# Kernel optimization log

Measured on AMD Instinct MI355X. Metric: run time of the kernel, lower is better.

Reference implementation:

```python
import jax, jax.numpy as jnp
import numpy as np

N, E, G = 100000, 1600000, 2048
F_NODE, F_EDGE, H, T = 32, 8, 128, 12


def _lin(key, fan_in, fan_out):
    k1, k2 = jax.random.split(key)
    s = 1.0 / np.sqrt(fan_in)
    W = jax.random.uniform(k1, (fan_in, fan_out), jnp.float32, -s, s)
    b = jax.random.uniform(k2, (fan_out,), jnp.float32, -s, s)
    return W, b


def setup_inputs() -> dict:
    key = jax.random.key(0)
    ks = jax.random.split(key, 12)
    x = jax.random.normal(ks[0], (N, F_NODE), jnp.float32)
    edge_index = jax.random.randint(ks[1], (2, E), 0, N, jnp.int64)
    edge_attr = jax.random.normal(ks[2], (E, F_EDGE), jnp.float32)
    batch = jnp.sort(jax.random.randint(ks[3], (N,), 0, G, jnp.int64))
    We1, be1 = _lin(ks[4], F_EDGE, F_NODE)   # conv1 edge lin: edge_dim -> in_channels
    W1a, b1a = _lin(ks[5], F_NODE, H)
    W1b, b1b = _lin(ks[6], H, H)
    We2, be2 = _lin(ks[7], F_EDGE, H)        # conv2 edge lin: edge_dim -> hidden
    W2a, b2a = _lin(ks[8], H, H)
    W2b, b2b = _lin(ks[9], H, H)
    Wl1, bl1 = _lin(ks[10], H, H)
    Wl2, bl2 = _lin(ks[11], H, T)
    return dict(x=x, edge_index=edge_index, edge_attr=edge_attr, batch=batch,
                We1=We1, be1=be1, W1a=W1a, b1a=b1a, W1b=W1b, b1b=b1b,
                We2=We2, be2=be2, W2a=W2a, b2a=b2a, W2b=W2b, b2b=b2b,
                Wl1=Wl1, bl1=bl1, Wl2=Wl2, bl2=bl2)


def _gine_conv(x, src, dst, edge_attr, We, be, Wa, ba, Wb, bb):
    # message: relu(x_j + Lin(edge_attr)), scatter-add to target, then MLP on (1+eps)*x + agg (eps=0)
    m = jax.nn.relu(x[src] + edge_attr @ We + be)          # [E, C]
    agg = jax.ops.segment_sum(m, dst, num_segments=x.shape[0])
    h = x + agg
    return jax.nn.elu(h @ Wa + ba) @ Wb + bb


def reference(x, edge_index, edge_attr, batch,
              We1, be1, W1a, b1a, W1b, b1b,
              We2, be2, W2a, b2a, W2b, b2b,
              Wl1, bl1, Wl2, bl2):
    src, dst = edge_index[0], edge_index[1]
    h = _gine_conv(x, src, dst, edge_attr, We1, be1, W1a, b1a, W1b, b1b)
    h = jax.nn.elu(h)  # dropout is identity at eval
    h = _gine_conv(h, src, dst, edge_attr, We2, be2, W2a, b2a, W2b, b2b)
    h = jax.nn.elu(h)
    hg = jax.ops.segment_sum(h, batch, num_segments=G)     # global add pool [G, H]
    hg = jax.nn.relu(hg @ Wl1 + bl1)
    return hg @ Wl2 + bl2                                  # [G, T]
```

## Files before the change

kernel.cpp:

```cpp
#include <hip/hip_runtime.h>
#include <math.h>

#define F_NODE 32
#define F_EDGE 8
#define HID 128
#define CAPB 6144

typedef __attribute__((ext_vector_type(2))) _Float16 f16x2;
typedef __attribute__((ext_vector_type(8))) _Float16 f16x8;
typedef __attribute__((ext_vector_type(4))) float f32x4;
typedef __attribute__((ext_vector_type(2))) float f32x2;

__device__ __forceinline__ float elu_f(float x) { return x > 0.f ? x : expf(x) - 1.f; }

__device__ __forceinline__ unsigned h2u(f16x2 h) { union { f16x2 h; unsigned u; } x; x.h = h; return x.u; }
__device__ __forceinline__ f16x2 u2h(unsigned u) { union { unsigned u; f16x2 h; } x; x.u = u; return x.h; }
__device__ __forceinline__ unsigned packh2(float lo, float hi) {
    f16x2 v; v.x = (_Float16)lo; v.y = (_Float16)hi; return h2u(v);
}
__device__ __forceinline__ unsigned short f2h_bits(float f) {
    _Float16 h = (_Float16)f; union { _Float16 h; unsigned short u; } x; x.h = h; return x.u;
}
__device__ __forceinline__ float hbits2f(unsigned short b) {
    union { unsigned short u; _Float16 h; } x; x.u = b; return (float)x.h;
}
__device__ __forceinline__ f16x8 frag_from(uint4 v) { union { uint4 u; f16x8 f; } x; x.u = v; return x.f; }
__device__ __forceinline__ f16x2 duph(f16x8 v, int k) { f16x2 d; d.x = v[k]; d.y = v[k]; return d; }

__global__ __launch_bounds__(256) void prep_kernel(
    const float* __restrict__ x, const float* __restrict__ ea,
    const int* __restrict__ dst,
    uint4* __restrict__ xh4, uint4* __restrict__ eab4,
    const float* __restrict__ W1a, const float* __restrict__ W1b,
    const float* __restrict__ W2a, const float* __restrict__ W2b,
    const float* __restrict__ Wl1, const float* __restrict__ Wl2,
    uint4* __restrict__ P1a, uint4* __restrict__ P1b,
    uint4* __restrict__ P2a, uint4* __restrict__ P2b,
    uint4* __restrict__ P3a, uint4* __restrict__ P3b,
    int* __restrict__ cnt, int nx, int ne2, int E)
{
    const int stride = gridDim.x * 256;
    const int tid = blockIdx.x * 256 + threadIdx.x;
    const float4* x4 = (const float4*)x;
    const float4* ea4 = (const float4*)ea;

    int nx4 = nx >> 2;
    for (int i = tid; i < nx4; i += stride) {
        float4 a = x4[i * 2], b = x4[i * 2 + 1];
        uint4 v;
        v.x = packh2(a.x, a.y);
        v.y = packh2(a.z, a.w);
        v.z = packh2(b.x, b.y);
        v.w = packh2(b.z, b.w);
        xh4[i] = v;
    }
    int ne8 = ne2 >> 2;
    for (int i = tid; i < ne8; i += stride) {
        float4 a = ea4[i * 2], b = ea4[i * 2 + 1];
        uint4 v;
        v.x = packh2(a.x, a.y);
        v.y = packh2(a.z, a.w);
        v.z = packh2(b.x, b.y);
        v.w = packh2(b.z, b.w);
        eab4[i] = v;
    }
    for (int f0 = tid; f0 < 8960; f0 += stride) {
        int f = f0;
        if (f >= 8704) {
            f -= 8704;
            int lane = f & 63;
            int ks = f >> 6;
            int col = lane & 15;
            int k0 = ks * 32 + (lane >> 4) * 8;
            float w[8];
#pragma unroll
            for (int j = 0; j < 8; ++j) w[j] = col < 12 ? Wl2[(size_t)(k0 + j) * 12 + col] : 0.f;
            uint4 v;
            v.x = packh2(w[0], w[1]);
            v.y = packh2(w[2], w[3]);
            v.z = packh2(w[4], w[5]);
            v.w = packh2(w[6], w[7]);
            P3b[f] = v;
            continue;
        }
        const float* W; uint4* P; int KS;
        if (f < 512)       { W = W1a; P = P1a; KS = 1; }
        else if (f < 2560) { W = W1b; P = P1b; KS = 4; f -= 512; }
        else if (f < 4608) { W = W2a; P = P2a; KS = 4; f -= 2560; }
        else if (f < 6656) { W = W2b; P = P2b; KS = 4; f -= 4608; }
        else               { W = Wl1; P = P3a; KS = 4; f -= 6656; }
        int lane = f & 63;
        int rem = f >> 6;
        int ks = rem % KS, ct = rem / KS;
        int col = ct * 16 + (lane & 15);
        int k0 = ks * 32 + (lane >> 4) * 8;
        float w[8];
#pragma unroll
        for (int j = 0; j < 8; ++j) w[j] = W[(size_t)(k0 + j) * HID + col];
        uint4 v;
        v.x = packh2(w[0], w[1]);
        v.y = packh2(w[2], w[3]);
        v.z = packh2(w[4], w[5]);
        v.w = packh2(w[6], w[7]);
        P[f] = v;
    }
    int e4 = E >> 2;
    const int4* dst4 = (const int4*)dst;
    for (int i = tid; i < e4; i += stride) {
        int4 d = dst4[i];
        atomicAdd(&cnt[d.x], 1);
        atomicAdd(&cnt[d.y], 1);
        atomicAdd(&cnt[d.z], 1);
        atomicAdd(&cnt[d.w], 1);
    }
    for (int i = e4 * 4 + tid; i < E; i += stride)
        atomicAdd(&cnt[dst[i]], 1);
}

__global__ void scan1_kernel(const int* __restrict__ in, int* __restrict__ out,
                             int* __restrict__ part, int n) {
    __shared__ int s[256];
    int t = threadIdx.x;
    int base = blockIdx.x * 1024 + t * 4;
    int v0 = base + 0 < n ? in[base + 0] : 0;
    int v1 = base + 1 < n ? in[base + 1] : 0;
    int v2 = base + 2 < n ? in[base + 2] : 0;
    int v3 = base + 3 < n ? in[base + 3] : 0;
    int tot = v0 + v1 + v2 + v3;
    s[t] = tot;
    __syncthreads();
    for (int off = 1; off < 256; off <<= 1) {
        int val = (t >= off) ? s[t - off] : 0;
        __syncthreads();
        s[t] += val;
        __syncthreads();
    }
    int pre = s[t] - tot;
    if (base + 0 < n) out[base + 0] = pre;
    if (base + 1 < n) out[base + 1] = pre + v0;
    if (base + 2 < n) out[base + 2] = pre + v0 + v1;
    if (base + 3 < n) out[base + 3] = pre + v0 + v1 + v2;
    if (t == 255) part[blockIdx.x] = s[255];
}

__global__ void scan2_kernel(int* part, int nb) {
    __shared__ int s[256];
    int t = threadIdx.x;
    int v = t < nb ? part[t] : 0;
    s[t] = v;
    __syncthreads();
    for (int off = 1; off < 256; off <<= 1) {
        int val = (t >= off) ? s[t - off] : 0;
        __syncthreads();
        s[t] += val;
        __syncthreads();
    }
    if (t < nb) part[t] = s[t] - v;
}

__global__ void scan3_kernel(int* __restrict__ out, const int* __restrict__ part,
                             int* __restrict__ curB, int* __restrict__ curFine,
                             int n, int total) {
    int i = blockIdx.x * blockDim.x + threadIdx.x;
    if (i < n) {
        int v = out[i] + part[i >> 10];
        out[i] = v;
        curFine[i] = v;
        if ((i & 255) == 0) curB[i >> 8] = v;
    }
    if (i == 0) out[n] = total;
}

__global__ __launch_bounds__(256) void binA_kernel(
    const int* __restrict__ dst, const int* __restrict__ src,
    int* __restrict__ curB, int2* __restrict__ tmp, int E, int NB)
{
    __shared__ int hist[512];
    __shared__ int basev[512];
    const int tid = threadIdx.x;
    const int base = blockIdx.x * 4096;
    for (int i = tid; i < NB; i += 256) hist[i] = 0;
    __syncthreads();
    int d[16];
#pragma unroll
    for (int k = 0; k < 16; ++k) {
        int e = base + k * 256 + tid;
        d[k] = (e < E) ? dst[e] : -1;
        if (d[k] >= 0) atomicAdd(&hist[d[k] >> 8], 1);
    }
    __syncthreads();
    for (int i = tid; i < NB; i += 256) {
        int c = hist[i];
        basev[i] = c > 0 ? atomicAdd(&curB[i], c) : 0;
        hist[i] = 0;
    }
    __syncthreads();
#pragma unroll
    for (int k = 0; k < 16; ++k) {
        int e = base + k * 256 + tid;
        if (d[k] >= 0) {
            int b = d[k] >> 8;
            int r = atomicAdd(&hist[b], 1);
            tmp[basev[b] + r] = make_int2(e | ((d[k] & 255) << 22), src[e]);
        }
    }
}

__global__ __launch_bounds__(256) void binB_kernel(
    const int2* __restrict__ tmp, const int* __restrict__ off,
    int* __restrict__ curFine, const uint4* __restrict__ eab4,
    int* __restrict__ srcarr, uint4* __restrict__ easrt, int N)
{
    __shared__ int ldsCur[256];
    __shared__ int2 stage[CAPB];
    const int b = blockIdx.x;
    const int tid = threadIdx.x;
    const int node0 = b << 8;
    const int nend = min(node0 + 256, N);
    const int base = off[node0];
    const int end = off[nend];
    const int S = end - base;
    if (S <= CAPB) {
        int node = node0 + tid;
        ldsCur[tid] = (node < nend ? off[node] : end) - base;
        __syncthreads();
        for (int j = tid; j < S; j += 256) {
            int2 rec = tmp[base + j];
            int dloc = ((unsigned)rec.x) >> 22;
            int slot = atomicAdd(&ldsCur[dloc], 1);
            stage[slot] = make_int2(rec.x & 0x3FFFFF, rec.y);
        }
        __syncthreads();
        for (int j = tid; j < S; j += 256) {
            int2 rec = stage[j];
            srcarr[base + j] = rec.y;
            easrt[base + j] = eab4[rec.x];
        }
    } else {
        for (int j = tid; j < S; j += 256) {
            int2 rec = tmp[base + j];
            int dloc = ((unsigned)rec.x) >> 22;
            int e = rec.x & 0x3FFFFF;
            int pos = atomicAdd(&curFine[node0 + dloc], 1);
            srcarr[pos] = rec.y;
            easrt[pos] = eab4[e];
        }
    }
}

__global__ __launch_bounds__(256) void agg1_kernel(
    const float* __restrict__ x, const unsigned* __restrict__ xh,
    const uint4* __restrict__ easrt,
    const float* __restrict__ We, const float* __restrict__ be,
    const int* __restrict__ off, const int* __restrict__ srcarr,
    unsigned* __restrict__ aggh, int N)
{
    int wave = (blockIdx.x * 256 + threadIdx.x) >> 6;
    if (wave >= N) return;
    int lane = threadIdx.x & 63;
    int fp = lane & 15, eg = lane >> 4;
    int j0 = fp * 2;
    f16x2 w2[F_EDGE];
#pragma unroll
    for (int k = 0; k < F_EDGE; ++k)
        w2[k] = u2h(packh2(We[k * F_NODE + j0], We[k * F_NODE + j0 + 1]));
    f16x2 bias2 = u2h(packh2(be[j0], be[j0 + 1]));
    f16x2 zero2 = u2h(0u);
    int i0 = __builtin_amdgcn_readfirstlane(off[wave]);
    int i1 = __builtin_amdgcn_readfirstlane(off[wave + 1]);
    float acc0 = 0.f, acc1 = 0.f;
    for (int i = i0; i < i1; i += 4) {
        int ii = i + eg;
        if (ii < i1) {
            int s = srcarr[ii];
            f16x8 ev = frag_from(easrt[ii]);
            f16x2 m = bias2 + u2h(xh[(size_t)s * 16 + fp]);
#pragma unroll
            for (int k = 0; k < F_EDGE; ++k)
                m = duph(ev, k) * w2[k] + m;
            m = __builtin_elementwise_max(m, zero2);
            acc0 += (float)m.x;
            acc1 += (float)m.y;
        }
    }
    acc0 += __shfl_xor(acc0, 16, 64);
    acc0 += __shfl_xor(acc0, 32, 64);
    acc1 += __shfl_xor(acc1, 16, 64);
    acc1 += __shfl_xor(acc1, 32, 64);
    if (eg == 0) {
        float2 xo = *(const float2*)&x[(size_t)wave * F_NODE + j0];
        aggh[(size_t)wave * 16 + fp] = packh2(xo.x + acc0, xo.y + acc1);
    }
}

__global__ __launch_bounds__(256) void agg2_kernel(
    const unsigned* __restrict__ hh, const unsigned short* __restrict__ h8,
    const uint4* __restrict__ easrt,
    const float* __restrict__ We, const float* __restrict__ be,
    const int* __restrict__ off, const int* __restrict__ srcarr,
    unsigned* __restrict__ aggh, int N)
{
    int wave = (blockIdx.x * 256 + threadIdx.x) >> 6;
    if (wave >= N) return;
    int lane = threadIdx.x & 63;
    int j0 = lane * 2;
    f16x2 w2[F_EDGE];
#pragma unroll
    for (int k = 0; k < F_EDGE; ++k)
        w2[k] = u2h(packh2(We[k * HID + j0], We[k * HID + j0 + 1]));
    f16x2 bias2 = u2h(packh2(be[j0], be[j0 + 1]));
    f16x2 zero2 = u2h(0u);
    int i0 = __builtin_amdgcn_readfirstlane(off[wave]);
    int i1 = __builtin_amdgcn_readfirstlane(off[wave + 1]);
    float acc0 = 0.f, acc1 = 0.f;
    int i = i0;
    for (; i + 7 < i1; i += 8) {
        int s[8];
        unsigned short u[8];
        f16x8 ev[8];
#pragma unroll
        for (int k = 0; k < 8; ++k) s[k] = srcarr[i + k];
#pragma unroll
        for (int k = 0; k < 8; ++k) u[k] = h8[(size_t)s[k] * 64 + lane];
#pragma unroll
        for (int k = 0; k < 8; ++k) ev[k] = frag_from(easrt[i + k]);
        f16x2 m[8];
#pragma unroll
        for (int k = 0; k < 8; ++k) {
            f32x2 f = __builtin_amdgcn_cvt_pk_f32_fp8((int)u[k], false);
            f16x2 hv; hv.x = (_Float16)f.x; hv.y = (_Float16)f.y;
            m[k] = bias2 + hv;
        }
#pragma unroll
        for (int kk = 0; kk < F_EDGE; ++kk) {
#pragma unroll
            for (int k = 0; k < 8; ++k)
                m[k] = duph(ev[k], kk) * w2[kk] + m[k];
        }
        f16x2 sm = __builtin_elementwise_max(m[0], zero2);
#pragma unroll
        for (int k = 1; k < 8; ++k) sm = sm + __builtin_elementwise_max(m[k], zero2);
        acc0 += (float)sm.x;
        acc1 += (float)sm.y;
    }
    for (; i < i1; ++i) {
        int s0 = srcarr[i];
        f16x8 e0 = frag_from(easrt[i]);
        f32x2 f = __builtin_amdgcn_cvt_pk_f32_fp8((int)h8[(size_t)s0 * 64 + lane], false);
        f16x2 hv; hv.x = (_Float16)f.x; hv.y = (_Float16)f.y;
        f16x2 m0 = bias2 + hv;
#pragma unroll
        for (int k = 0; k < F_EDGE; ++k)
            m0 = duph(e0, k) * w2[k] + m0;
        m0 = __builtin_elementwise_max(m0, zero2);
        acc0 += (float)m0.x;
        acc1 += (float)m0.y;
    }
    f16x2 self = u2h(hh[(size_t)wave * 64 + lane]);
    aggh[(size_t)wave * 64 + lane] = packh2((float)self.x + acc0, (float)self.y + acc1);
}

__device__ __forceinline__ void put_tile_elu_h(unsigned short* t, f32x4 v, int rbase, int c, int stride) {
#pragma unroll
    for (int j = 0; j < 4; ++j)
        t[(rbase + j) * stride + c] = f2h_bits(elu_f(v[j]));
}
__device__ __forceinline__ void put_tile_relu_h(unsigned short* t, f32x4 v, int rbase, int c, int stride) {
#pragma unroll
    for (int j = 0; j < 4; ++j)
        t[(rbase + j) * stride + c] = f2h_bits(fmaxf(v[j], 0.f));
}

template <int K, bool POOL, bool DUP8>
__global__ __launch_bounds__(256) void mlp_mfma_kernel(
    const uint4* __restrict__ inb,
    const uint4* __restrict__ WaP, const float* __restrict__ ba,
    const uint4* __restrict__ WbP, const float* __restrict__ bb,
    uint4* __restrict__ outb, unsigned* __restrict__ out8,
    const int* __restrict__ batch, float* __restrict__ hg,
    int nrows)
{
    constexpr int KS_A = K / 32;
    constexpr int SA = K + 8;
    constexpr int ST = HID + 8;
    constexpr int STF = HID + 4;
    __shared__ __align__(16) unsigned short a_s[32 * SA];
    __shared__ __align__(16) unsigned short t_s[32 * ST];
    __shared__ float p_s[POOL ? 32 * STF : 1];
    __shared__ int batch_s[POOL ? 32 : 1];

    const int tid = threadIdx.x;
    const int row0 = blockIdx.x * 32;

    constexpr int Q = K / 8;
    for (int idx = tid; idx < 32 * Q; idx += 256) {
        int r = idx / Q, q = idx % Q;
        uint4 v = make_uint4(0, 0, 0, 0);
        if (row0 + r < nrows) v = inb[(size_t)(row0 + r) * Q + q];
        *(uint4*)&a_s[r * SA + q * 8] = v;
    }
    if (POOL && tid < 32)
        batch_s[tid] = (row0 + tid < nrows) ? batch[row0 + tid] : -1;
    __syncthreads();

    const int lane = tid & 63;
    const int w = tid >> 6;
    const int rb = w >> 1;
    const int cg = (w & 1) * 4;
    const int cf = lane & 15;
    const int g = lane >> 4;
    const int arow = rb * 16 + cf;

    f32x4 acc0, acc1, acc2, acc3;
    {
        float c0 = ba[(cg + 0) * 16 + cf], c1 = ba[(cg + 1) * 16 + cf];
        float c2 = ba[(cg + 2) * 16 + cf], c3 = ba[(cg + 3) * 16 + cf];
        acc0 = (f32x4){c0, c0, c0, c0};
        acc1 = (f32x4){c1, c1, c1, c1};
        acc2 = (f32x4){c2, c2, c2, c2};
        acc3 = (f32x4){c3, c3, c3, c3};
    }
#pragma unroll
    for (int ks = 0; ks < KS_A; ++ks) {
        f16x8 a = *(const f16x8*)&a_s[arow * SA + ks * 32 + g * 8];
        acc0 = __builtin_amdgcn_mfma_f32_16x16x32_f16(a, frag_from(WaP[((cg + 0) * KS_A + ks) * 64 + lane]), acc0, 0, 0, 0);
        acc1 = __builtin_amdgcn_mfma_f32_16x16x32_f16(a, frag_from(WaP[((cg + 1) * KS_A + ks) * 64 + lane]), acc1, 0, 0, 0);
        acc2 = __builtin_amdgcn_mfma_f32_16x16x32_f16(a, frag_from(WaP[((cg + 2) * KS_A + ks) * 64 + lane]), acc2, 0, 0, 0);
        acc3 = __builtin_amdgcn_mfma_f32_16x16x32_f16(a, frag_from(WaP[((cg + 3) * KS_A + ks) * 64 + lane]), acc3, 0, 0, 0);
    }
    {
        int rbase = rb * 16 + g * 4;
        put_tile_elu_h(t_s, acc0, rbase, (cg + 0) * 16 + cf, ST);
        put_tile_elu_h(t_s, acc1, rbase, (cg + 1) * 16 + cf, ST);
        put_tile_elu_h(t_s, acc2, rbase, (cg + 2) * 16 + cf, ST);
        put_tile_elu_h(t_s, acc3, rbase, (cg + 3) * 16 + cf, ST);
    }
    __syncthreads();

    {
        float c0 = bb[(cg + 0) * 16 + cf], c1 = bb[(cg + 1) * 16 + cf];
        float c2 = bb[(cg + 2) * 16 + cf], c3 = bb[(cg + 3) * 16 + cf];
        acc0 = (f32x4){c0, c0, c0, c0};
        acc1 = (f32x4){c1, c1, c1, c1};
        acc2 = (f32x4){c2, c2, c2, c2};
        acc3 = (f32x4){c3, c3, c3, c3};
    }
#pragma unroll
    for (int ks = 0; ks < 4; ++ks) {
        f16x8 a = *(const f16x8*)&t_s[arow * ST + ks * 32 + g * 8];
        acc0 = __builtin_amdgcn_mfma_f32_16x16x32_f16(a, frag_from(WbP[((cg + 0) * 4 + ks) * 64 + lane]), acc0, 0, 0, 0);
        acc1 = __builtin_amdgcn_mfma_f32_16x16x32_f16(a, frag_from(WbP[((cg + 1) * 4 + ks) * 64 + lane]), acc1, 0, 0, 0);
        acc2 = __builtin_amdgcn_mfma_f32_16x16x32_f16(a, frag_from(WbP[((cg + 2) * 4 + ks) * 64 + lane]), acc2, 0, 0, 0);
        acc3 = __builtin_amdgcn_mfma_f32_16x16x32_f16(a, frag_from(WbP[((cg + 3) * 4 + ks) * 64 + lane]), acc3, 0, 0, 0);
    }

    if (POOL) {
        int rbase = rb * 16 + g * 4;
#pragma unroll
        for (int j = 0; j < 4; ++j) {
            p_s[(rbase + j) * STF + (cg + 0) * 16 + cf] = elu_f(acc0[j]);
            p_s[(rbase + j) * STF + (cg + 1) * 16 + cf] = elu_f(acc1[j]);
            p_s[(rbase + j) * STF + (cg + 2) * 16 + cf] = elu_f(acc2[j]);
            p_s[(rbase + j) * STF + (cg + 3) * 16 + cf] = elu_f(acc3[j]);
        }
        __syncthreads();
        int f = tid & 127, grp = tid >> 7;
        float acc = 0.f;
        int cur = -1;
#pragma unroll 4
        for (int r = 0; r < 16; ++r) {
            int rr = grp * 16 + r;
            int b = batch_s[rr];
            if (b >= 0) {
                if (b != cur) {
                    if (cur >= 0) atomicAdd(&hg[(size_t)cur * HID + f], acc);
                    acc = 0.f;
                    cur = b;
                }
                acc += p_s[rr * STF + f];
            }
        }
        if (cur >= 0) atomicAdd(&hg[(size_t)cur * HID + f], acc);
    } else {
        __syncthreads();
        int rbase = rb * 16 + g * 4;
        put_tile_elu_h(t_s, acc0, rbase, (cg + 0) * 16 + cf, ST);
        put_tile_elu_h(t_s, acc1, rbase, (cg + 1) * 16 + cf, ST);
        put_tile_elu_h(t_s, acc2, rbase, (cg + 2) * 16 + cf, ST);
        put_tile_elu_h(t_s, acc3, rbase, (cg + 3) * 16 + cf, ST);
        __syncthreads();
        for (int idx = tid; idx < 32 * 16; idx += 256) {
            int r = idx >> 4, q = idx & 15;
            if (row0 + r < nrows)
                outb[(size_t)(row0 + r) * 16 + q] = *(const uint4*)&t_s[r * ST + q * 8];
        }
        if (DUP8) {
            for (int idx = tid; idx < 32 * 32; idx += 256) {
                int r = idx >> 5, q = idx & 31;
                if (row0 + r < nrows) {
                    float f0 = hbits2f(t_s[r * ST + q * 4 + 0]);
                    float f1 = hbits2f(t_s[r * ST + q * 4 + 1]);
                    float f2 = hbits2f(t_s[r * ST + q * 4 + 2]);
                    float f3 = hbits2f(t_s[r * ST + q * 4 + 3]);
                    int u = __builtin_amdgcn_cvt_pk_fp8_f32(f0, f1, 0, false);
                    u = __builtin_amdgcn_cvt_pk_fp8_f32(f2, f3, u, true);
                    out8[(size_t)(row0 + r) * 32 + q] = (unsigned)u;
                }
            }
        }
    }
}

__global__ __launch_bounds__(256) void head_mfma_kernel(
    const float* __restrict__ hg,
    const uint4* __restrict__ Wl1P, const float* __restrict__ bl1,
    const uint4* __restrict__ Wl2P, const float* __restrict__ bl2,
    float* __restrict__ out, int G)
{
    constexpr int ST = HID + 8;
    __shared__ __align__(16) unsigned short a_s[32 * ST];
    __shared__ __align__(16) unsigned short t_s[32 * ST];

    const int tid = threadIdx.x;
    const int row0 = blockIdx.x * 32;

    for (int idx = tid; idx < 32 * HID; idx += 256) {
        int r = idx >> 7, c = idx & 127;
        float v = (row0 + r < G) ? hg[(size_t)(row0 + r) * HID + c] : 0.f;
        a_s[r * ST + c] = f2h_bits(v);
    }
    __syncthreads();

    const int lane = tid & 63;
    const int w = tid >> 6;
    const int rb = w >> 1;
    const int cg = (w & 1) * 4;
    const int cf = lane & 15;
    const int g = lane >> 4;
    const int arow = rb * 16 + cf;

    f32x4 acc0, acc1, acc2, acc3;
    {
        float c0 = bl1[(cg + 0) * 16 + cf], c1 = bl1[(cg + 1) * 16 + cf];
        float c2 = bl1[(cg + 2) * 16 + cf], c3 = bl1[(cg + 3) * 16 + cf];
        acc0 = (f32x4){c0, c0, c0, c0};
        acc1 = (f32x4){c1, c1, c1, c1};
        acc2 = (f32x4){c2, c2, c2, c2};
        acc3 = (f32x4){c3, c3, c3, c3};
    }
#pragma unroll
    for (int ks = 0; ks < 4; ++ks) {
        f16x8 a = *(const f16x8*)&a_s[arow * ST + ks * 32 + g * 8];
        acc0 = __builtin_amdgcn_mfma_f32_16x16x32_f16(a, frag_from(Wl1P[((cg + 0) * 4 + ks) * 64 + lane]), acc0, 0, 0, 0);
        acc1 = __builtin_amdgcn_mfma_f32_16x16x32_f16(a, frag_from(Wl1P[((cg + 1) * 4 + ks) * 64 + lane]), acc1, 0, 0, 0);
        acc2 = __builtin_amdgcn_mfma_f32_16x16x32_f16(a, frag_from(Wl1P[((cg + 2) * 4 + ks) * 64 + lane]), acc2, 0, 0, 0);
        acc3 = __builtin_amdgcn_mfma_f32_16x16x32_f16(a, frag_from(Wl1P[((cg + 3) * 4 + ks) * 64 + lane]), acc3, 0, 0, 0);
    }
    {
        int rbase = rb * 16 + g * 4;
        put_tile_relu_h(t_s, acc0, rbase, (cg + 0) * 16 + cf, ST);
        put_tile_relu_h(t_s, acc1, rbase, (cg + 1) * 16 + cf, ST);
        put_tile_relu_h(t_s, acc2, rbase, (cg + 2) * 16 + cf, ST);
        put_tile_relu_h(t_s, acc3, rbase, (cg + 3) * 16 + cf, ST);
    }
    __syncthreads();

    if ((w & 1) == 0) {
        float c0 = cf < 12 ? bl2[cf] : 0.f;
        f32x4 acc = (f32x4){c0, c0, c0, c0};
#pragma unroll
        for (int ks = 0; ks < 4; ++ks) {
            f16x8 a = *(const f16x8*)&t_s[arow * ST + ks * 32 + g * 8];
            acc = __builtin_amdgcn_mfma_f32_16x16x32_f16(a, frag_from(Wl2P[ks * 64 + lane]), acc, 0, 0, 0);
        }
        if (cf < 12) {
            int rbase = rb * 16 + g * 4;
#pragma unroll
            for (int j = 0; j < 4; ++j) {
                int row = row0 + rbase + j;
                if (row < G) out[(size_t)row * 12 + cf] = acc[j];
            }
        }
    }
}

extern "C" void kernel_launch(void* const* d_in, const int* in_sizes, int n_in,
                              void* d_out, int out_size, void* d_ws, size_t ws_size,
                              hipStream_t stream)
{
    const float* x    = (const float*)d_in[0];
    const int*   ei   = (const int*)d_in[1];
    const float* ea   = (const float*)d_in[2];
    const int*   batch = (const int*)d_in[3];
    const float* We1 = (const float*)d_in[4];
    const float* be1 = (const float*)d_in[5];
    const float* W1a = (const float*)d_in[6];
    const float* b1a = (const float*)d_in[7];
    const float* W1b = (const float*)d_in[8];
    const float* b1b = (const float*)d_in[9];
    const float* We2 = (const float*)d_in[10];
    const float* be2 = (const float*)d_in[11];
    const float* W2a = (const float*)d_in[12];
    const float* b2a = (const float*)d_in[13];
    const float* W2b = (const float*)d_in[14];
    const float* b2b = (const float*)d_in[15];
    const float* Wl1 = (const float*)d_in[16];
    const float* bl1 = (const float*)d_in[17];
    const float* Wl2 = (const float*)d_in[18];
    const float* bl2 = (const float*)d_in[19];
    float* out = (float*)d_out;

    const int N = in_sizes[0] / F_NODE;
    const int E = in_sizes[1] / 2;
    const int G = out_size / 12;
    const int NB = (N + 255) >> 8;

    const int* srcp = ei;
    const int* dstp = ei + E;

    char* wsb = (char*)d_ws;
    auto alloc = [&](size_t bytes) -> char* {
        char* p = wsb;
        wsb += (bytes + 15) & ~(size_t)15;
        return p;
    };
    int* cnt     = (int*)alloc((size_t)N * 4);
    int* off     = (int*)alloc((size_t)(N + 1) * 4);
    int* part    = (int*)alloc(256 * 4);
    int* curB    = (int*)alloc(512 * 4);
    int* curFine = (int*)alloc((size_t)N * 4);
    int2* tmp    = (int2*)alloc((size_t)E * 8);
    unsigned short* h8 = (unsigned short*)tmp;
    int* srcarr  = (int*)alloc((size_t)E * 4);
    uint4* easrt = (uint4*)alloc((size_t)E * 16);
    unsigned* xh   = (unsigned*)alloc((size_t)N * 16 * 4);
    unsigned* eab  = (unsigned*)alloc((size_t)E * 4 * 4);
    unsigned* agg2h = eab;
    unsigned* agg1h = (unsigned*)alloc((size_t)N * 16 * 4);
    unsigned* h1h   = (unsigned*)alloc((size_t)N * 64 * 4);
    float* hg  = (float*)alloc((size_t)G * HID * 4);
    uint4* P1a = (uint4*)alloc(512 * 16);
    uint4* P1b = (uint4*)alloc(2048 * 16);
    uint4* P2a = (uint4*)alloc(2048 * 16);
    uint4* P2b = (uint4*)alloc(2048 * 16);
    uint4* P3a = (uint4*)alloc(2048 * 16);
    uint4* P3b = (uint4*)alloc(256 * 16);

    (void)hipMemsetAsync(cnt, 0, (size_t)N * sizeof(int), stream);
    (void)hipMemsetAsync(hg, 0, (size_t)G * HID * sizeof(float), stream);

    hipLaunchKernelGGL(prep_kernel, dim3(2048), dim3(256), 0, stream,
                       x, ea, dstp, (uint4*)xh, (uint4*)eab, W1a, W1b, W2a, W2b, Wl1, Wl2,
                       P1a, P1b, P2a, P2b, P3a, P3b, cnt, N * 16, E * 4, E);
    int nscan = (N + 1023) / 1024;
    hipLaunchKernelGGL(scan1_kernel, dim3(nscan), dim3(256), 0, stream, cnt, off, part, N);
    hipLaunchKernelGGL(scan2_kernel, dim3(1), dim3(256), 0, stream, part, nscan);
    hipLaunchKernelGGL(scan3_kernel, dim3((N + 255) / 256), dim3(256), 0, stream,
                       off, part, curB, curFine, N, E);
    hipLaunchKernelGGL(binA_kernel, dim3((E + 4095) / 4096), dim3(256), 0, stream,
                       dstp, srcp, curB, tmp, E, NB);
    hipLaunchKernelGGL(binB_kernel, dim3(NB), dim3(256), 0, stream,
                       tmp, off, curFine, (const uint4*)eab, srcarr, easrt, N);

    hipLaunchKernelGGL(agg1_kernel, dim3((N + 3) / 4), dim3(256), 0, stream,
                       x, xh, easrt, We1, be1, off, srcarr, agg1h, N);
    hipLaunchKernelGGL((mlp_mfma_kernel<F_NODE, false, true>), dim3((N + 31) / 32), dim3(256), 0, stream,
                       (const uint4*)agg1h, P1a, b1a, P1b, b1b, (uint4*)h1h, (unsigned*)h8,
                       (const int*)nullptr, (float*)nullptr, N);

    hipLaunchKernelGGL(agg2_kernel, dim3((N + 3) / 4), dim3(256), 0, stream,
                       h1h, h8, easrt, We2, be2, off, srcarr, agg2h, N);
    hipLaunchKernelGGL((mlp_mfma_kernel<HID, true, false>), dim3((N + 31) / 32), dim3(256), 0, stream,
                       (const uint4*)agg2h, P2a, b2a, P2b, b2b, (uint4*)nullptr, (unsigned*)nullptr,
                       batch, hg, N);

    hipLaunchKernelGGL(head_mfma_kernel, dim3((G + 31) / 32), dim3(256), 0, stream,
                       hg, P3a, bl1, P3b, bl2, out, G);
}
```

Measured before the change: 361.9 us.

## Replace per-node global count and 3-pass scan with bucket histogram and local scan

Edge counting now uses per-block LDS histograms over 256-node buckets, merged into a small global bucket-count array, in place of global atomics per node. The three scan kernels become one single-thread scan over about 400 buckets. Per-node offsets are now computed inside binB with a local histogram and block scan, and binB drops the LDS staging buffer and the fallback path. This removes 1.6M global atomics and two launches, but binB now reads tmp twice and writes scattered output directly to global memory.

```diff
diff --git a/kernel.cpp b/kernel.cpp
--- a/kernel.cpp
+++ b/kernel.cpp
@@ -4,7 +4,6 @@
 #define F_NODE 32
 #define F_EDGE 8
 #define HID 128
-#define CAPB 6144
 
 typedef __attribute__((ext_vector_type(2))) _Float16 f16x2;
 typedef __attribute__((ext_vector_type(8))) _Float16 f16x8;
@@ -37,12 +36,16 @@
     uint4* __restrict__ P1a, uint4* __restrict__ P1b,
     uint4* __restrict__ P2a, uint4* __restrict__ P2b,
     uint4* __restrict__ P3a, uint4* __restrict__ P3b,
-    int* __restrict__ cnt, int nx, int ne2, int E)
+    int* __restrict__ cbkt, int nx, int ne2, int E, int NB)
 {
     const int stride = gridDim.x * 256;
     const int tid = blockIdx.x * 256 + threadIdx.x;
     const float4* x4 = (const float4*)x;
     const float4* ea4 = (const float4*)ea;
+
+    __shared__ int chist[512];
+    for (int i = threadIdx.x; i < 512; i += 256) chist[i] = 0;
+    __syncthreads();
 
     int nx4 = nx >> 2;
     for (int i = tid; i < nx4; i += stride) {
@@ -108,67 +111,32 @@
     const int4* dst4 = (const int4*)dst;
     for (int i = tid; i < e4; i += stride) {
         int4 d = dst4[i];
-        atomicAdd(&cnt[d.x], 1);
-        atomicAdd(&cnt[d.y], 1);
-        atomicAdd(&cnt[d.z], 1);
-        atomicAdd(&cnt[d.w], 1);
+        atomicAdd(&chist[d.x >> 8], 1);
+        atomicAdd(&chist[d.y >> 8], 1);
+        atomicAdd(&chist[d.z >> 8], 1);
+        atomicAdd(&chist[d.w >> 8], 1);
     }
     for (int i = e4 * 4 + tid; i < E; i += stride)
-        atomicAdd(&cnt[dst[i]], 1);
-}
-
-__global__ void scan1_kernel(const int* __restrict__ in, int* __restrict__ out,
-                             int* __restrict__ part, int n) {
-    __shared__ int s[256];
-    int t = threadIdx.x;
-    int base = blockIdx.x * 1024 + t * 4;
-    int v0 = base + 0 < n ? in[base + 0] : 0;
-    int v1 = base + 1 < n ? in[base + 1] : 0;
-    int v2 = base + 2 < n ? in[base + 2] : 0;
-    int v3 = base + 3 < n ? in[base + 3] : 0;
-    int tot = v0 + v1 + v2 + v3;
-    s[t] = tot;
-    __syncthreads();
-    for (int off = 1; off < 256; off <<= 1) {
-        int val = (t >= off) ? s[t - off] : 0;
-        __syncthreads();
-        s[t] += val;
-        __syncthreads();
-    }
-    int pre = s[t] - tot;
-    if (base + 0 < n) out[base + 0] = pre;
-    if (base + 1 < n) out[base + 1] = pre + v0;
-    if (base + 2 < n) out[base + 2] = pre + v0 + v1;
-    if (base + 3 < n) out[base + 3] = pre + v0 + v1 + v2;
-    if (t == 255) part[blockIdx.x] = s[255];
-}
-
-__global__ void scan2_kernel(int* part, int nb) {
-    __shared__ int s[256];
-    int t = threadIdx.x;
-    int v = t < nb ? part[t] : 0;
-    s[t] = v;
-    __syncthreads();
-    for (int off = 1; off < 256; off <<= 1) {
-        int val = (t >= off) ? s[t - off] : 0;
-        __syncthreads();
-        s[t] += val;
-        __syncthreads();
-    }
-    if (t < nb) part[t] = s[t] - v;
-}
-
-__global__ void scan3_kernel(int* __restrict__ out, const int* __restrict__ part,
-                             int* __restrict__ curB, int* __restrict__ curFine,
-                             int n, int total) {
-    int i = blockIdx.x * blockDim.x + threadIdx.x;
-    if (i < n) {
-        int v = out[i] + part[i >> 10];
-        out[i] = v;
-        curFine[i] = v;
-        if ((i & 255) == 0) curB[i >> 8] = v;
-    }
-    if (i == 0) out[n] = total;
+        atomicAdd(&chist[dst[i] >> 8], 1);
+    __syncthreads();
+    for (int i = threadIdx.x; i < NB; i += 256) {
+        int c = chist[i];
+        if (c) atomicAdd(&cbkt[i], c);
+    }
+}
+
+__global__ void scanB_kernel(const int* __restrict__ cbkt,
+                             int* __restrict__ bucketOff, int* __restrict__ curB,
+                             int NB, int E) {
+    if (threadIdx.x == 0 && blockIdx.x == 0) {
+        int acc = 0;
+        for (int i = 0; i < NB; ++i) {
+            bucketOff[i] = acc;
+            curB[i] = acc;
+            acc += cbkt[i];
+        }
+        bucketOff[NB] = E;
+    }
 }
 
 __global__ __launch_bounds__(256) void binA_kernel(
@@ -207,44 +175,48 @@
 }
 
 __global__ __launch_bounds__(256) void binB_kernel(
-    const int2* __restrict__ tmp, const int* __restrict__ off,
-    int* __restrict__ curFine, const uint4* __restrict__ eab4,
-    int* __restrict__ srcarr, uint4* __restrict__ easrt, int N)
-{
-    __shared__ int ldsCur[256];
-    __shared__ int2 stage[CAPB];
+    const int2* __restrict__ tmp, const int* __restrict__ bucketOff,
+    const uint4* __restrict__ eab4,
+    int* __restrict__ off, int* __restrict__ srcarr, uint4* __restrict__ easrt,
+    int N, int E, int NB)
+{
+    __shared__ int hist[256];
+    __shared__ int ss[256];
     const int b = blockIdx.x;
     const int tid = threadIdx.x;
     const int node0 = b << 8;
-    const int nend = min(node0 + 256, N);
-    const int base = off[node0];
-    const int end = off[nend];
+    const int base = bucketOff[b];
+    const int end = bucketOff[b + 1];
     const int S = end - base;
-    if (S <= CAPB) {
-        int node = node0 + tid;
-        ldsCur[tid] = (node < nend ? off[node] : end) - base;
+
+    hist[tid] = 0;
+    __syncthreads();
+    for (int j = tid; j < S; j += 256) {
+        int2 rec = tmp[base + j];
+        atomicAdd(&hist[((unsigned)rec.x) >> 22], 1);
+    }
+    __syncthreads();
+    int v = hist[tid];
+    ss[tid] = v;
+    __syncthreads();
+    for (int o = 1; o < 256; o <<= 1) {
+        int val = (tid >= o) ? ss[tid - o] : 0;
         __syncthreads();
-        for (int j = tid; j < S; j += 256) {
-            int2 rec = tmp[base + j];
-            int dloc = ((unsigned)rec.x) >> 22;
-            int slot = atomicAdd(&ldsCur[dloc], 1);
-            stage[slot] = make_int2(rec.x & 0x3FFFFF, rec.y);
-        }
+        ss[tid] += val;
         __syncthreads();
-        for (int j = tid; j < S; j += 256) {
-            int2 rec = stage[j];
-            srcarr[base + j] = rec.y;
-            easrt[base + j] = eab4[rec.x];
-        }
-    } else {
-        for (int j = tid; j < S; j += 256) {
-            int2 rec = tmp[base + j];
-            int dloc = ((unsigned)rec.x) >> 22;
-            int e = rec.x & 0x3FFFFF;
-            int pos = atomicAdd(&curFine[node0 + dloc], 1);
-            srcarr[pos] = rec.y;
-            easrt[pos] = eab4[e];
-        }
+    }
+    int excl = ss[tid] - v;
+    int node = node0 + tid;
+    if (node < N) off[node] = base + excl;
+    if (b == NB - 1 && tid == 0) off[N] = E;
+    hist[tid] = excl;
+    __syncthreads();
+    for (int j = tid; j < S; j += 256) {
+        int2 rec = tmp[base + j];
+        int dloc = ((unsigned)rec.x) >> 22;
+        int slot = base + atomicAdd(&hist[dloc], 1);
+        srcarr[slot] = rec.y;
+        easrt[slot] = eab4[rec.x & 0x3FFFFF];
     }
 }
 
@@ -624,15 +596,14 @@
         wsb += (bytes + 15) & ~(size_t)15;
         return p;
     };
-    int* cnt     = (int*)alloc((size_t)N * 4);
-    int* off     = (int*)alloc((size_t)(N + 1) * 4);
-    int* part    = (int*)alloc(256 * 4);
-    int* curB    = (int*)alloc(512 * 4);
-    int* curFine = (int*)alloc((size_t)N * 4);
-    int2* tmp    = (int2*)alloc((size_t)E * 8);
+    int* cbkt      = (int*)alloc(512 * 4);
+    int* bucketOff = (int*)alloc(513 * 4);
+    int* curB      = (int*)alloc(512 * 4);
+    int* off       = (int*)alloc((size_t)(N + 1) * 4);
+    int2* tmp      = (int2*)alloc((size_t)E * 8);
     unsigned short* h8 = (unsigned short*)tmp;
-    int* srcarr  = (int*)alloc((size_t)E * 4);
-    uint4* easrt = (uint4*)alloc((size_t)E * 16);
+    int* srcarr    = (int*)alloc((size_t)E * 4);
+    uint4* easrt   = (uint4*)alloc((size_t)E * 16);
     unsigned* xh   = (unsigned*)alloc((size_t)N * 16 * 4);
     unsigned* eab  = (unsigned*)alloc((size_t)E * 4 * 4);
     unsigned* agg2h = eab;
@@ -646,21 +617,17 @@
     uint4* P3a = (uint4*)alloc(2048 * 16);
     uint4* P3b = (uint4*)alloc(256 * 16);
 
-    (void)hipMemsetAsync(cnt, 0, (size_t)N * sizeof(int), stream);
+    (void)hipMemsetAsync(cbkt, 0, 512 * sizeof(int), stream);
     (void)hipMemsetAsync(hg, 0, (size_t)G * HID * sizeof(float), stream);
 
     hipLaunchKernelGGL(prep_kernel, dim3(2048), dim3(256), 0, stream,
                        x, ea, dstp, (uint4*)xh, (uint4*)eab, W1a, W1b, W2a, W2b, Wl1, Wl2,
-                       P1a, P1b, P2a, P2b, P3a, P3b, cnt, N * 16, E * 4, E);
-    int nscan = (N + 1023) / 1024;
-    hipLaunchKernelGGL(scan1_kernel, dim3(nscan), dim3(256), 0, stream, cnt, off, part, N);
-    hipLaunchKernelGGL(scan2_kernel, dim3(1), dim3(256), 0, stream, part, nscan);
-    hipLaunchKernelGGL(scan3_kernel, dim3((N + 255) / 256), dim3(256), 0, stream,
-                       off, part, curB, curFine, N, E);
+                       P1a, P1b, P2a, P2b, P3a, P3b, cbkt, N * 16, E * 4, E, NB);
+    hipLaunchKernelGGL(scanB_kernel, dim3(1), dim3(64), 0, stream, cbkt, bucketOff, curB, NB, E);
     hipLaunchKernelGGL(binA_kernel, dim3((E + 4095) / 4096), dim3(256), 0, stream,
                        dstp, srcp, curB, tmp, E, NB);
     hipLaunchKernelGGL(binB_kernel, dim3(NB), dim3(256), 0, stream,
-                       tmp, off, curFine, (const uint4*)eab, srcarr, easrt, N);
+                       tmp, bucketOff, (const uint4*)eab, off, srcarr, easrt, N, E, NB);
 
     hipLaunchKernelGGL(agg1_kernel, dim3((N + 3) / 4), dim3(256), 0, stream,
                        x, xh, easrt, We1, be1, off, srcarr, agg1h, N);
```

Result: no change. 359.6 us (-0.6%).
